# Optimization experiments

Hardware: AMD Instinct MI355X
Metric: run time of the kernel (lower is better)

The kernel has to match this reference:

```python
import jax, jax.numpy as jnp
import numpy as np

B, E, C, Fdim, T = 8, 36, 4, 32, 2048
EDGE_DIM, NODE_DIM, NUM_NODES, NUM_CLASSES = 64, 128, 12, 9
# edges: all (i, j) with i in 0..5, j in 6..11, in loop order
U = np.repeat(np.arange(6), 6)
V = np.tile(np.arange(6, 12), 6)


def _p(key, shape, scale=0.05):
    return jax.random.normal(key, shape, jnp.float32) * scale


def setup_inputs():
    ks = iter(jax.random.split(jax.random.key(0), 64))
    nxt = lambda: next(ks)
    inp = {}
    inp["x"] = jax.random.normal(nxt(), (B, E, C, Fdim, T), jnp.float32)
    inp["conv1_w"] = _p(nxt(), (16, C, 3, 3)); inp["conv1_b"] = _p(nxt(), (16,))
    inp["bn1_s"] = jnp.ones((16,)); inp["bn1_b"] = jnp.zeros((16,))
    inp["bn1_m"] = jnp.zeros((16,)); inp["bn1_v"] = jnp.ones((16,))
    inp["se1_w1"] = _p(nxt(), (4, 16)); inp["se1_b1"] = _p(nxt(), (4,))
    inp["se1_w2"] = _p(nxt(), (16, 4)); inp["se1_b2"] = _p(nxt(), (16,))
    inp["conv2_w"] = _p(nxt(), (32, 16, 3, 3)); inp["conv2_b"] = _p(nxt(), (32,))
    inp["bn2_s"] = jnp.ones((32,)); inp["bn2_b"] = jnp.zeros((32,))
    inp["bn2_m"] = jnp.zeros((32,)); inp["bn2_v"] = jnp.ones((32,))
    inp["se2_w1"] = _p(nxt(), (8, 32)); inp["se2_b1"] = _p(nxt(), (8,))
    inp["se2_w2"] = _p(nxt(), (32, 8)); inp["se2_b2"] = _p(nxt(), (32,))
    inp["conv3_w"] = _p(nxt(), (64, 32, 3, 3)); inp["conv3_b"] = _p(nxt(), (64,))
    inp["bn3_s"] = jnp.ones((64,)); inp["bn3_b"] = jnp.zeros((64,))
    inp["bn3_m"] = jnp.zeros((64,)); inp["bn3_v"] = jnp.ones((64,))
    inp["edge_fc_w"] = _p(nxt(), (EDGE_DIM, 64)); inp["edge_fc_b"] = _p(nxt(), (EDGE_DIM,))
    inp["edge_w"] = _p(nxt(), (E,), 1.0)  # learnable_edge_weights
    inp["e2n_w"] = _p(nxt(), (NODE_DIM, EDGE_DIM)); inp["e2n_b"] = _p(nxt(), (NODE_DIM,))
    inp["attn1_w"] = _p(nxt(), (NODE_DIM // 2, NODE_DIM)); inp["attn1_b"] = _p(nxt(), (NODE_DIM // 2,))
    inp["attn2_w"] = _p(nxt(), (1, NODE_DIM // 2))
    inp["cls_w"] = _p(nxt(), (NUM_CLASSES, NODE_DIM)); inp["cls_b"] = _p(nxt(), (NUM_CLASSES,))
    inp["reg_w"] = _p(nxt(), (3, NODE_DIM)); inp["reg_b"] = _p(nxt(), (3,))
    return inp


def _conv(x, w, b, stride):
    y = jax.lax.conv_general_dilated(x, w, window_strides=stride,
        padding=[(1, 1), (1, 1)], dimension_numbers=("NCHW", "OIHW", "NCHW"))
    return y + b[None, :, None, None]


def _bn(x, s, b, m, v):
    # eval-mode BatchNorm2d (running stats)
    inv = s * jax.lax.rsqrt(v + 1e-5)
    return (x - m[None, :, None, None]) * inv[None, :, None, None] + b[None, :, None, None]


def _maxpool2(x):
    return jax.lax.reduce_window(x, -jnp.inf, jax.lax.max,
        (1, 1, 2, 2), (1, 1, 2, 2), "VALID")


def _se(x, w1, b1, w2, b2):
    y = x.mean(axis=(2, 3))                      # [N, C]
    y = jax.nn.relu(y @ w1.T + b1)
    y = jax.nn.sigmoid(y @ w2.T + b2)
    return x * y[:, :, None, None]


def _forward(x, conv1_w, conv1_b, bn1_s, bn1_b, bn1_m, bn1_v,
             se1_w1, se1_b1, se1_w2, se1_b2,
             conv2_w, conv2_b, bn2_s, bn2_b, bn2_m, bn2_v,
             se2_w1, se2_b1, se2_w2, se2_b2,
             conv3_w, conv3_b, bn3_s, bn3_b, bn3_m, bn3_v,
             edge_fc_w, edge_fc_b, edge_w, e2n_w, e2n_b,
             attn1_w, attn1_b, attn2_w, cls_w, cls_b, reg_w, reg_b):
    h = x.reshape(B * E, C, Fdim, T)
    h = jax.nn.relu(_bn(_conv(h, conv1_w, conv1_b, (1, 2)), bn1_s, bn1_b, bn1_m, bn1_v))
    h = _se(_maxpool2(h), se1_w1, se1_b1, se1_w2, se1_b2)
    h = jax.nn.relu(_bn(_conv(h, conv2_w, conv2_b, (1, 2)), bn2_s, bn2_b, bn2_m, bn2_v))
    h = _se(_maxpool2(h), se2_w1, se2_b1, se2_w2, se2_b2)
    h = jax.nn.relu(_bn(_conv(h, conv3_w, conv3_b, (1, 2)), bn3_s, bn3_b, bn3_m, bn3_v))
    h = h.mean(axis=(2, 3))                      # AdaptiveAvgPool2d(1) -> [B*E, 64]
    edge_feat = jax.nn.relu(h @ edge_fc_w.T + edge_fc_b).reshape(B, E, EDGE_DIM)

    # spatial GNN: weighted edge feats scatter-added to both endpoints
    w = jax.nn.softplus(edge_w)[None, :, None]   # [1, E, 1]
    wef = edge_feat * w                          # [B, E, D]
    node = jnp.zeros((B, NUM_NODES, EDGE_DIM), edge_feat.dtype)
    node = node.at[:, U].add(wef).at[:, V].add(wef)
    node = jax.nn.relu(node @ e2n_w.T + e2n_b)   # [B, 12, NODE_DIM]

    # attention pooling
    scores = jnp.tanh(node @ attn1_w.T + attn1_b) @ attn2_w.T   # [B, 12, 1]
    aw = jax.nn.softmax(scores, axis=1)
    ea = aw[:, U, 0] * aw[:, V, 0]               # [B, E]
    ea = ea / (ea.sum(axis=1, keepdims=True) + 1e-8)
    g = (node * aw).sum(axis=1)                  # [B, NODE_DIM]
    return (g @ reg_w.T + reg_b, g @ cls_w.T + cls_b, ea)


def reference(x, conv1_w, conv1_b, bn1_s, bn1_b, bn1_m, bn1_v,
              se1_w1, se1_b1, se1_w2, se1_b2,
              conv2_w, conv2_b, bn2_s, bn2_b, bn2_m, bn2_v,
              se2_w1, se2_b1, se2_w2, se2_b2,
              conv3_w, conv3_b, bn3_s, bn3_b, bn3_m, bn3_v,
              edge_fc_w, edge_fc_b, edge_w, e2n_w, e2n_b,
              attn1_w, attn1_b, attn2_w, cls_w, cls_b, reg_w, reg_b):
    return _forward(x, conv1_w, conv1_b, bn1_s, bn1_b, bn1_m, bn1_v,
                    se1_w1, se1_b1, se1_w2, se1_b2,
                    conv2_w, conv2_b, bn2_s, bn2_b, bn2_m, bn2_v,
                    se2_w1, se2_b1, se2_w2, se2_b2,
                    conv3_w, conv3_b, bn3_s, bn3_b, bn3_m, bn3_v,
                    edge_fc_w, edge_fc_b, edge_w, e2n_w, e2n_b,
                    attn1_w, attn1_b, attn2_w, cls_w, cls_b, reg_w, reg_b)
```

## Files before the change

kernel.cpp:

```cpp
#include <hip/hip_runtime.h>
#include <math.h>


#define GLOAD_LDS(src, dst) \
  __builtin_amdgcn_global_load_lds( \
      (const __attribute__((address_space(1))) void*)(src), \
      (__attribute__((address_space(3))) void*)(dst), 16, 0, 0)

__global__ __launch_bounds__(256) void k_conv1(
    const float* __restrict__ x, const float* __restrict__ w,
    const float* __restrict__ cb, const float* __restrict__ bs,
    const float* __restrict__ bb, const float* __restrict__ bm,
    const float* __restrict__ bv,
    float* __restrict__ h1, float* __restrict__ sesum)
{
  int bid = blockIdx.x;
  int colq = bid & 3, chunk = (bid >> 2) & 1, n = bid >> 3;
  __shared__ float tile[4][6][520];
  __shared__ float wl[4][3][3][16];
  __shared__ float bi[16];

  const float* xn = x + (size_t)n * 4 * 32 * 2048;
  const int cbase = colq * 512;
  int tid = threadIdx.x;
  for (int i = tid; i < 576; i += 256) {
    int co = i / 36, r = i % 36, ci = r / 9, kk = r % 9;
    float s = bs[co] * rsqrtf(bv[co] + 1e-5f);
    wl[ci][kk / 3][kk % 3][co] = w[i] * s;
  }
  if (tid < 16) {
    int c = tid;
    float s = bs[c] * rsqrtf(bv[c] + 1e-5f);
    bi[c] = bb[c] + (cb[c] - bm[c]) * s;
  }
  int wv = tid >> 6, l = tid & 63;
  const int P0 = chunk * 8;
  {
#pragma unroll
    for (int j = 0; j < 8; j++) {
      int idx = wv * 8 + j;
      int ci = idx >> 3, rowidx = (idx >> 1) & 3, half = idx & 1;
      int ih = 2 * P0 - 1 + rowidx;
      int slot = ((ih % 6) + 6) % 6;
      int ihc = min(max(ih, 0), 31);
      const float* src =
          xn + ((size_t)ci * 32 + ihc) * 2048 + cbase + half * 256 + 4 * l;
      GLOAD_LDS(src, &tile[ci][slot][4 + half * 256 + 4 * l]);
    }
    if (tid < 16) {
      int ri = tid & 3, ci = tid >> 2;
      int ih2 = 2 * P0 - 1 + ri, slot2 = ((ih2 % 6) + 6) % 6;
      int ihc2 = min(max(ih2, 0), 31);
      tile[ci][slot2][3] =
          colq ? xn[((size_t)ci * 32 + ihc2) * 2048 + cbase - 1] : 0.f;
    }
  }
  __syncthreads();

  int cog = tid >> 7, tl = tid & 127;
  int cob = cog * 8;
  float sloc[8] = {0.f, 0.f, 0.f, 0.f, 0.f, 0.f, 0.f, 0.f};

#pragma unroll 1
  for (int pl = 0; pl < 8; pl++) {
    int p = P0 + pl;
    if (pl < 7) {
#pragma unroll
      for (int j = 0; j < 4; j++) {
        int idx = wv * 4 + j;
        int ci = idx >> 2, rsel = (idx >> 1) & 1, half = idx & 1;
        int ih = 2 * p + 3 + rsel;
        int slot = ih % 6;
        int ihc = min(ih, 31);
        const float* src =
            xn + ((size_t)ci * 32 + ihc) * 2048 + cbase + half * 256 + 4 * l;
        GLOAD_LDS(src, &tile[ci][slot][4 + half * 256 + 4 * l]);
      }
      if (tid < 8) {
        int rs2 = tid & 1, ci2 = tid >> 1;
        int ih2 = 2 * p + 3 + rs2, slot2 = ih2 % 6, ihc2 = min(ih2, 31);
        tile[ci2][slot2][3] =
            colq ? xn[((size_t)ci2 * 32 + ihc2) * 2048 + cbase - 1] : 0.f;
      }
    }
    float acc[2][2][8];
#pragma unroll
    for (int cr = 0; cr < 2; cr++)
#pragma unroll
      for (int cc = 0; cc < 2; cc++)
#pragma unroll
        for (int k = 0; k < 8; k++) acc[cr][cc][k] = 0.f;
    const bool ok0 = (p > 0), ok3 = (p < 15);
    int slots[4];
#pragma unroll
    for (int r = 0; r < 4; r++) {
      int ih = 2 * p - 1 + r;
      slots[r] = ((ih % 6) + 6) % 6;
    }
#pragma unroll 1
    for (int ci = 0; ci < 4; ci++) {
      float strip[4][5];
#pragma unroll
      for (int r = 0; r < 4; r++) {
        bool ok = (r == 0) ? ok0 : ((r == 3) ? ok3 : true);
        if (ok) {
          float4 vA = *reinterpret_cast<const float4*>(&tile[ci][slots[r]][4 * tl]);
          float4 vB = *reinterpret_cast<const float4*>(&tile[ci][slots[r]][4 * tl + 4]);
          strip[r][0] = vA.w;
          strip[r][1] = vB.x; strip[r][2] = vB.y; strip[r][3] = vB.z; strip[r][4] = vB.w;
        } else {
          strip[r][0] = strip[r][1] = strip[r][2] = strip[r][3] = strip[r][4] = 0.f;
        }
      }
#pragma unroll
      for (int kh = 0; kh < 3; kh++) {
#pragma unroll
        for (int kw = 0; kw < 3; kw++) {
          const float4* wp = reinterpret_cast<const float4*>(&wl[ci][kh][kw][cob]);
          float4 w0 = wp[0], w1 = wp[1];
          float wr[8] = {w0.x, w0.y, w0.z, w0.w, w1.x, w1.y, w1.z, w1.w};
#pragma unroll
          for (int cr = 0; cr < 2; cr++) {
            float v0 = strip[cr + kh][kw], v1 = strip[cr + kh][2 + kw];
#pragma unroll
            for (int k = 0; k < 8; k++) {
              acc[cr][0][k] = fmaf(v0, wr[k], acc[cr][0][k]);
              acc[cr][1][k] = fmaf(v1, wr[k], acc[cr][1][k]);
            }
          }
        }
      }
    }
    int pc = colq * 128 + tl;
#pragma unroll
    for (int k = 0; k < 8; k++) {
      float m = fmaxf(fmaxf(acc[0][0][k], acc[0][1][k]),
                      fmaxf(acc[1][0][k], acc[1][1][k]));
      float po = fmaxf(m + bi[cob + k], 0.f);
      h1[(((size_t)n * 16 + cob + k) * 16 + p) * 512 + pc] = po;
      sloc[k] += po;
    }
    __syncthreads();
  }
#pragma unroll
  for (int k = 0; k < 8; k++) {
    float v = sloc[k];
    for (int off = 32; off; off >>= 1) v += __shfl_down(v, off);
    if (l == 0) atomicAdd(&sesum[n * 16 + cob + k], v);
  }
}

__global__ void k_se(const float* __restrict__ sesum, int C, int Cr, float invcnt,
                     const float* __restrict__ w1, const float* __restrict__ b1,
                     const float* __restrict__ w2, const float* __restrict__ b2,
                     float* __restrict__ s)
{
  int n = blockIdx.x * blockDim.x + threadIdx.x;
  if (n >= 288) return;
  float y[32], t[8];
  for (int c = 0; c < C; c++) y[c] = sesum[n * C + c] * invcnt;
  for (int r = 0; r < Cr; r++) {
    float a = b1[r];
    for (int c = 0; c < C; c++) a += y[c] * w1[r * C + c];
    t[r] = fmaxf(a, 0.f);
  }
  for (int c = 0; c < C; c++) {
    float a = b2[c];
    for (int r = 0; r < Cr; r++) a += t[r] * w2[c * Cr + r];
    s[n * C + c] = 1.f / (1.f + expf(-a));
  }
}

__global__ __launch_bounds__(256) void k_conv2(
    const float* __restrict__ h1, const float* __restrict__ w,
    const float* __restrict__ cb, const float* __restrict__ bs,
    const float* __restrict__ bb, const float* __restrict__ bm,
    const float* __restrict__ bv,
    const float* __restrict__ s1,
    float* __restrict__ h2, float* __restrict__ sesum)
{
  int bid = blockIdx.x;
  int ph = bid & 7, n = bid >> 3;
  __shared__ float tile[2][2][4][520];
  __shared__ float wl[16][3][3][32];
  __shared__ float bi[32];

  const float* s1n = s1 + n * 16;
  for (int i = threadIdx.x; i < 4608; i += 256) {
    int co = i / 144, r = i % 144, ci = r / 9, kk = r % 9;
    float s = bs[co] * rsqrtf(bv[co] + 1e-5f);
    wl[ci][kk / 3][kk % 3][co] = w[i] * s * s1n[ci];
  }
  if (threadIdx.x < 32) {
    int c = threadIdx.x;
    float s = bs[c] * rsqrtf(bv[c] + 1e-5f);
    bi[c] = bb[c] + (cb[c] - bm[c]) * s;
  }
  if (threadIdx.x < 64) {
    int b = threadIdx.x >> 5, ci = (threadIdx.x >> 4) & 1,
        r = (threadIdx.x >> 2) & 3, k = threadIdx.x & 3;
    tile[b][ci][r][k] = 0.f;
  }

  const float* hn = h1 + (size_t)n * 16 * 16 * 512;
  int wv = threadIdx.x >> 6, l = threadIdx.x & 63;

  auto stage = [&](int c, int b) {
#pragma unroll
    for (int j = 0; j < 4; j++) {
      int idx = 4 * wv + j;
      int ci_l = idx >> 3, r = (idx >> 1) & 3, half = idx & 1;
      int ci = 2 * c + ci_l;
      int ih = min(max(2 * ph - 1 + r, 0), 15);
      const float* src = hn + ((size_t)ci * 16 + ih) * 512 + half * 256 + 4 * l;
      GLOAD_LDS(src, &tile[b][ci_l][r][4 + half * 256 + 4 * l]);
    }
  };

  stage(0, 0);
  __syncthreads();

  int cog = threadIdx.x >> 7, tl = threadIdx.x & 127;
  int cob = cog * 16;
  const bool ok0 = (ph > 0), ok3 = (ph < 7);
  float acc[2][2][16];
#pragma unroll
  for (int cr = 0; cr < 2; cr++)
#pragma unroll
    for (int cc = 0; cc < 2; cc++)
#pragma unroll
      for (int k = 0; k < 16; k++) acc[cr][cc][k] = 0.f;

#pragma unroll 1
  for (int c = 0; c < 8; c++) {
    if (c < 7) stage(c + 1, (c + 1) & 1);
    const int b = c & 1;
#pragma unroll 1
    for (int ci_l = 0; ci_l < 2; ci_l++) {
      int cg = 2 * c + ci_l;
      float strip[4][5];
#pragma unroll
      for (int r = 0; r < 4; r++) {
        bool ok = (r == 0) ? ok0 : ((r == 3) ? ok3 : true);
        if (ok) {
          float4 vA = *reinterpret_cast<const float4*>(&tile[b][ci_l][r][4 * tl]);
          float4 vB = *reinterpret_cast<const float4*>(&tile[b][ci_l][r][4 * tl + 4]);
          strip[r][0] = vA.w;
          strip[r][1] = vB.x; strip[r][2] = vB.y; strip[r][3] = vB.z; strip[r][4] = vB.w;
        } else {
          strip[r][0] = strip[r][1] = strip[r][2] = strip[r][3] = strip[r][4] = 0.f;
        }
      }
#pragma unroll
      for (int kh = 0; kh < 3; kh++) {
#pragma unroll
        for (int kw = 0; kw < 3; kw++) {
          const float4* wp = reinterpret_cast<const float4*>(&wl[cg][kh][kw][cob]);
          float4 w0 = wp[0], w1 = wp[1], w2 = wp[2], w3 = wp[3];
          float wr[16] = {w0.x, w0.y, w0.z, w0.w, w1.x, w1.y, w1.z, w1.w,
                          w2.x, w2.y, w2.z, w2.w, w3.x, w3.y, w3.z, w3.w};
#pragma unroll
          for (int cr = 0; cr < 2; cr++) {
            float v0 = strip[cr + kh][kw], v1 = strip[cr + kh][2 + kw];
#pragma unroll
            for (int k = 0; k < 16; k++) {
              acc[cr][0][k] = fmaf(v0, wr[k], acc[cr][0][k]);
              acc[cr][1][k] = fmaf(v1, wr[k], acc[cr][1][k]);
            }
          }
        }
      }
    }
    if (c < 7) __syncthreads();
  }

#pragma unroll
  for (int k = 0; k < 16; k++) {
    float m = fmaxf(fmaxf(acc[0][0][k], acc[0][1][k]),
                    fmaxf(acc[1][0][k], acc[1][1][k]));
    float po = fmaxf(m + bi[cob + k], 0.f);
    h2[(((size_t)n * 32 + cob + k) * 8 + ph) * 128 + tl] = po;
    float v = po;
    for (int off = 32; off; off >>= 1) v += __shfl_down(v, off);
    if (l == 0) atomicAdd(&sesum[n * 32 + cob + k], v);
  }
}

__global__ __launch_bounds__(256) void k_conv3(
    const float* __restrict__ h2, const float* __restrict__ w,
    const float* __restrict__ cb, const float* __restrict__ bs,
    const float* __restrict__ bb, const float* __restrict__ bm,
    const float* __restrict__ bv,
    const float* __restrict__ s2, float* __restrict__ h3)
{
  int bid = blockIdx.x;
  int n = bid >> 2, cog = bid & 3;
  int hh = threadIdx.x >> 5, t = threadIdx.x & 31;
  __shared__ float tile[8][8][128];
  __shared__ float wl[32][3][3][16];
  __shared__ float bi[16];
  __shared__ float red[4][16];
  const float* s2n = s2 + n * 32;
  for (int i = threadIdx.x; i < 4608; i += 256) {
    int k = i / 288, r = i % 288, ci = r / 9, kk = r % 9;
    int co = cog * 16 + k;
    float s = bs[co] * rsqrtf(bv[co] + 1e-5f);
    wl[ci][kk / 3][kk % 3][k] = w[(size_t)co * 288 + r] * s * s2n[ci];
  }
  if (threadIdx.x < 16) {
    int c = cog * 16 + threadIdx.x;
    float s = bs[c] * rsqrtf(bv[c] + 1e-5f);
    bi[threadIdx.x] = bb[c] + (cb[c] - bm[c]) * s;
  }
  const float* hn = h2 + (size_t)n * 32 * 8 * 128;
  int wv = threadIdx.x >> 6, l = threadIdx.x & 63;
  const int aoff = t ? 4 * t - 4 : 0;
  float acc[2][16];
#pragma unroll
  for (int cc = 0; cc < 2; cc++)
#pragma unroll
    for (int k = 0; k < 16; k++) acc[cc][k] = 0.f;

#pragma unroll 1
  for (int c = 0; c < 4; c++) {
    for (int i = 0; i < 8; i++) {
      int pair = wv * 8 + i;
      int ci_l = pair >> 2, r2 = (pair & 3) * 2;
      int ci = c * 8 + ci_l;
      const float* src = hn + ((size_t)ci * 8 + r2) * 128 + 4 * l;
      GLOAD_LDS(src, &tile[ci_l][r2][4 * l]);
    }
    __syncthreads();
#pragma unroll 1
    for (int ci_l = 0; ci_l < 8; ci_l++) {
      int cg = c * 8 + ci_l;
      float strip[3][5];
#pragma unroll
      for (int r = 0; r < 3; r++) {
        int ih = hh - 1 + r;
        if (ih >= 0 && ih <= 7) {
          float4 vB = *reinterpret_cast<const float4*>(&tile[ci_l][ih][4 * t]);
          float4 vA = *reinterpret_cast<const float4*>(&tile[ci_l][ih][aoff]);
          strip[r][0] = t ? vA.w : 0.f;
          strip[r][1] = vB.x; strip[r][2] = vB.y; strip[r][3] = vB.z; strip[r][4] = vB.w;
        } else {
          strip[r][0] = strip[r][1] = strip[r][2] = strip[r][3] = strip[r][4] = 0.f;
        }
      }
#pragma unroll
      for (int kh = 0; kh < 3; kh++) {
#pragma unroll
        for (int kw = 0; kw < 3; kw++) {
          const float4* wp = reinterpret_cast<const float4*>(&wl[cg][kh][kw][0]);
          float4 w0 = wp[0], w1 = wp[1], w2 = wp[2], w3 = wp[3];
          float wr[16] = {w0.x, w0.y, w0.z, w0.w, w1.x, w1.y, w1.z, w1.w,
                          w2.x, w2.y, w2.z, w2.w, w3.x, w3.y, w3.z, w3.w};
          float v0 = strip[kh][kw], v1 = strip[kh][2 + kw];
#pragma unroll
          for (int k = 0; k < 16; k++) {
            acc[0][k] = fmaf(v0, wr[k], acc[0][k]);
            acc[1][k] = fmaf(v1, wr[k], acc[1][k]);
          }
        }
      }
    }
    __syncthreads();
  }
#pragma unroll
  for (int k = 0; k < 16; k++)
    acc[0][k] = fmaxf(acc[0][k] + bi[k], 0.f) + fmaxf(acc[1][k] + bi[k], 0.f);
#pragma unroll
  for (int k = 0; k < 16; k++) {
    float v = acc[0][k];
    for (int off = 32; off; off >>= 1) v += __shfl_down(v, off);
    if (l == 0) red[wv][k] = v;
  }
  __syncthreads();
  if (threadIdx.x < 16) {
    int k = threadIdx.x;
    float tt = red[0][k] + red[1][k] + red[2][k] + red[3][k];
    h3[n * 64 + cog * 16 + k] = tt * (1.f / 512.f);
  }
}

__global__ __launch_bounds__(256) void k_head(
    const float* __restrict__ h3,
    const float* __restrict__ efw, const float* __restrict__ efb,
    const float* __restrict__ ew,
    const float* __restrict__ e2nw, const float* __restrict__ e2nb,
    const float* __restrict__ a1w, const float* __restrict__ a1b,
    const float* __restrict__ a2w,
    const float* __restrict__ clsw, const float* __restrict__ clsb,
    const float* __restrict__ regw, const float* __restrict__ regb,
    float* __restrict__ out)
{
  int b = blockIdx.x;
  int tid = threadIdx.x;
  __shared__ float ef[36][64];
  __shared__ float nin[12][64];
  __shared__ float nd[12][128];
  __shared__ float tmp[12][64];
  __shared__ float spw[36], aw[12], scv[12], g[128], ea[36];
  if (tid < 36) {
    float xw = ew[tid];
    spw[tid] = (xw > 20.f) ? xw : log1pf(expf(xw));
  }
  __syncthreads();
  for (int idx = tid; idx < 36 * 64; idx += 256) {
    int e = idx >> 6, d = idx & 63;
    const float* hr = h3 + (size_t)(b * 36 + e) * 64;
    const float* wr = efw + d * 64;
    float a = efb[d];
    for (int k = 0; k < 64; k++) a += hr[k] * wr[k];
    ef[e][d] = fmaxf(a, 0.f) * spw[e];
  }
  __syncthreads();
  for (int idx = tid; idx < 12 * 64; idx += 256) {
    int j = idx >> 6, d = idx & 63;
    float a = 0.f;
    if (j < 6) { for (int i = 0; i < 6; i++) a += ef[j * 6 + i][d]; }
    else       { for (int i = 0; i < 6; i++) a += ef[i * 6 + (j - 6)][d]; }
    nin[j][d] = a;
  }
  __syncthreads();
  for (int idx = tid; idx < 12 * 128; idx += 256) {
    int j = idx >> 7, d = idx & 127;
    const float* wr = e2nw + d * 64;
    float a = e2nb[d];
    for (int k = 0; k < 64; k++) a += nin[j][k] * wr[k];
    nd[j][d] = fmaxf(a, 0.f);
  }
  __syncthreads();
  for (int idx = tid; idx < 12 * 64; idx += 256) {
    int j = idx >> 6, hh = idx & 63;
    const float* wr = a1w + hh * 128;
    float a = a1b[hh];
    for (int k = 0; k < 128; k++) a += nd[j][k] * wr[k];
    tmp[j][hh] = tanhf(a) * a2w[hh];
  }
  __syncthreads();
  if (tid < 12) {
    float a = 0.f;
    for (int h = 0; h < 64; h++) a += tmp[tid][h];
    scv[tid] = a;
  }
  __syncthreads();
  if (tid == 0) {
    float m = scv[0];
    for (int j = 1; j < 12; j++) m = fmaxf(m, scv[j]);
    float s = 0.f;
    for (int j = 0; j < 12; j++) { float z = expf(scv[j] - m); aw[j] = z; s += z; }
    float inv = 1.f / s;
    for (int j = 0; j < 12; j++) aw[j] *= inv;
    float rs = 0.f;
    for (int e = 0; e < 36; e++) { float r = aw[e / 6] * aw[6 + e % 6]; ea[e] = r; rs += r; }
    float inv2 = 1.f / (rs + 1e-8f);
    for (int e = 0; e < 36; e++) ea[e] *= inv2;
  }
  __syncthreads();
  if (tid < 36) out[96 + b * 36 + tid] = ea[tid];
  if (tid < 128) {
    float a = 0.f;
    for (int j = 0; j < 12; j++) a += nd[j][tid] * aw[j];
    g[tid] = a;
  }
  __syncthreads();
  if (tid < 3) {
    const float* wr = regw + tid * 128;
    float a = regb[tid];
    for (int k = 0; k < 128; k++) a += g[k] * wr[k];
    out[b * 3 + tid] = a;
  }
  if (tid >= 64 && tid < 73) {
    int i = tid - 64;
    const float* wr = clsw + i * 128;
    float a = clsb[i];
    for (int k = 0; k < 128; k++) a += g[k] * wr[k];
    out[24 + b * 9 + i] = a;
  }
}

extern "C" void kernel_launch(void* const* d_in, const int* in_sizes, int n_in,
                              void* d_out, int out_size, void* d_ws, size_t ws_size,
                              hipStream_t stream) {
  const float* x      = (const float*)d_in[0];
  const float* c1w    = (const float*)d_in[1];
  const float* c1b    = (const float*)d_in[2];
  const float* bn1s   = (const float*)d_in[3];
  const float* bn1b   = (const float*)d_in[4];
  const float* bn1m   = (const float*)d_in[5];
  const float* bn1v   = (const float*)d_in[6];
  const float* se1w1  = (const float*)d_in[7];
  const float* se1b1  = (const float*)d_in[8];
  const float* se1w2  = (const float*)d_in[9];
  const float* se1b2  = (const float*)d_in[10];
  const float* c2w    = (const float*)d_in[11];
  const float* c2b    = (const float*)d_in[12];
  const float* bn2s   = (const float*)d_in[13];
  const float* bn2b   = (const float*)d_in[14];
  const float* bn2m   = (const float*)d_in[15];
  const float* bn2v   = (const float*)d_in[16];
  const float* se2w1  = (const float*)d_in[17];
  const float* se2b1  = (const float*)d_in[18];
  const float* se2w2  = (const float*)d_in[19];
  const float* se2b2  = (const float*)d_in[20];
  const float* c3w    = (const float*)d_in[21];
  const float* c3b    = (const float*)d_in[22];
  const float* bn3s   = (const float*)d_in[23];
  const float* bn3b   = (const float*)d_in[24];
  const float* bn3m   = (const float*)d_in[25];
  const float* bn3v   = (const float*)d_in[26];
  const float* efw    = (const float*)d_in[27];
  const float* efb    = (const float*)d_in[28];
  const float* ew     = (const float*)d_in[29];
  const float* e2nw   = (const float*)d_in[30];
  const float* e2nb   = (const float*)d_in[31];
  const float* a1w    = (const float*)d_in[32];
  const float* a1b    = (const float*)d_in[33];
  const float* a2w    = (const float*)d_in[34];
  const float* clsw   = (const float*)d_in[35];
  const float* clsb   = (const float*)d_in[36];
  const float* regw   = (const float*)d_in[37];
  const float* regb   = (const float*)d_in[38];

  float* ws = (float*)d_ws;
  float* h1     = ws;
  float* h2     = h1 + 37748736;
  float* sesum1 = h2 + 9437184;
  float* s1     = sesum1 + 4608;
  float* sesum2 = s1 + 4608;
  float* s2     = sesum2 + 9216;
  float* h3     = s2 + 9216;

  hipMemsetAsync(sesum1, 0, 4608 * sizeof(float), stream);
  hipMemsetAsync(sesum2, 0, 9216 * sizeof(float), stream);

  k_conv1<<<288 * 8, 256, 0, stream>>>(x, c1w, c1b, bn1s, bn1b, bn1m, bn1v, h1, sesum1);
  k_se<<<5, 64, 0, stream>>>(sesum1, 16, 4, 1.f / 8192.f, se1w1, se1b1, se1w2, se1b2, s1);
  k_conv2<<<288 * 8, 256, 0, stream>>>(h1, c2w, c2b, bn2s, bn2b, bn2m, bn2v, s1, h2, sesum2);
  k_se<<<5, 64, 0, stream>>>(sesum2, 32, 8, 1.f / 1024.f, se2w1, se2b1, se2w2, se2b2, s2);
  k_conv3<<<288 * 4, 256, 0, stream>>>(h2, c3w, c3b, bn3s, bn3b, bn3m, bn3v, s2, h3);
  k_head<<<8, 256, 0, stream>>>(h3, efw, efb, ew, e2nw, e2nb, a1w, a1b, a2w,
                                clsw, clsb, regw, regb, (float*)d_out);
}
```

Baseline: 521.4 us.

## Precompute folded conv weights in global memory and read them as uniform scalar loads

Moves the BN/SE weight folding for conv1 and conv2 out of every block into small prologue kernels that write the folded weights to workspace once (per batch for conv2). The conv kernels then read the weights directly from global memory through a wave-uniform base (readfirstlane) so the compiler can use scalar loads, instead of staging them into LDS. This removes per-block redundant folding work and LDS weight traffic, and frees LDS, at the cost of two extra kernel launches and reliance on the scalar cache for weight reads.

```diff
diff --git a/kernel.cpp b/kernel.cpp
--- a/kernel.cpp
+++ b/kernel.cpp
@@ -7,8 +7,32 @@
       (const __attribute__((address_space(1))) void*)(src), \
       (__attribute__((address_space(3))) void*)(dst), 16, 0, 0)
 
+__global__ void k_fold1(const float* __restrict__ w, const float* __restrict__ bs,
+                        const float* __restrict__ bv, float* __restrict__ wf1)
+{
+  int i = blockIdx.x * blockDim.x + threadIdx.x;
+  if (i < 576) {
+    int co = i / 36, r = i % 36;
+    float s = bs[co] * rsqrtf(bv[co] + 1e-5f);
+    wf1[r * 16 + co] = w[i] * s;
+  }
+}
+
+__global__ void k_fold2(const float* __restrict__ w, const float* __restrict__ bs,
+                        const float* __restrict__ bv, const float* __restrict__ s1,
+                        float* __restrict__ wf2)
+{
+  int n = blockIdx.x;
+  const float* s1n = s1 + n * 16;
+  for (int i = threadIdx.x; i < 4608; i += 256) {
+    int co = i / 144, r = i % 144, ci = r / 9;
+    float s = bs[co] * rsqrtf(bv[co] + 1e-5f);
+    wf2[(size_t)n * 4608 + r * 32 + co] = w[i] * s * s1n[ci];
+  }
+}
+
 __global__ __launch_bounds__(256) void k_conv1(
-    const float* __restrict__ x, const float* __restrict__ w,
+    const float* __restrict__ x, const float* __restrict__ wf1,
     const float* __restrict__ cb, const float* __restrict__ bs,
     const float* __restrict__ bb, const float* __restrict__ bm,
     const float* __restrict__ bv,
@@ -17,17 +41,11 @@
   int bid = blockIdx.x;
   int colq = bid & 3, chunk = (bid >> 2) & 1, n = bid >> 3;
   __shared__ float tile[4][6][520];
-  __shared__ float wl[4][3][3][16];
   __shared__ float bi[16];
 
   const float* xn = x + (size_t)n * 4 * 32 * 2048;
   const int cbase = colq * 512;
   int tid = threadIdx.x;
-  for (int i = tid; i < 576; i += 256) {
-    int co = i / 36, r = i % 36, ci = r / 9, kk = r % 9;
-    float s = bs[co] * rsqrtf(bv[co] + 1e-5f);
-    wl[ci][kk / 3][kk % 3][co] = w[i] * s;
-  }
   if (tid < 16) {
     int c = tid;
     float s = bs[c] * rsqrtf(bv[c] + 1e-5f);
@@ -58,7 +76,7 @@
   __syncthreads();
 
   int cog = tid >> 7, tl = tid & 127;
-  int cob = cog * 8;
+  const int cobu = __builtin_amdgcn_readfirstlane(cog * 8);
   float sloc[8] = {0.f, 0.f, 0.f, 0.f, 0.f, 0.f, 0.f, 0.f};
 
 #pragma unroll 1
@@ -112,12 +130,13 @@
           strip[r][0] = strip[r][1] = strip[r][2] = strip[r][3] = strip[r][4] = 0.f;
         }
       }
+      const float* wci = wf1 + ci * 9 * 16 + cobu;
 #pragma unroll
       for (int kh = 0; kh < 3; kh++) {
 #pragma unroll
         for (int kw = 0; kw < 3; kw++) {
-          const float4* wp = reinterpret_cast<const float4*>(&wl[ci][kh][kw][cob]);
-          float4 w0 = wp[0], w1 = wp[1];
+          const float4* wq = reinterpret_cast<const float4*>(wci + (kh * 3 + kw) * 16);
+          float4 w0 = wq[0], w1 = wq[1];
           float wr[8] = {w0.x, w0.y, w0.z, w0.w, w1.x, w1.y, w1.z, w1.w};
 #pragma unroll
           for (int cr = 0; cr < 2; cr++) {
@@ -136,8 +155,8 @@
     for (int k = 0; k < 8; k++) {
       float m = fmaxf(fmaxf(acc[0][0][k], acc[0][1][k]),
                       fmaxf(acc[1][0][k], acc[1][1][k]));
-      float po = fmaxf(m + bi[cob + k], 0.f);
-      h1[(((size_t)n * 16 + cob + k) * 16 + p) * 512 + pc] = po;
+      float po = fmaxf(m + bi[cobu + k], 0.f);
+      h1[(((size_t)n * 16 + cobu + k) * 16 + p) * 512 + pc] = po;
       sloc[k] += po;
     }
     __syncthreads();
@@ -146,7 +165,7 @@
   for (int k = 0; k < 8; k++) {
     float v = sloc[k];
     for (int off = 32; off; off >>= 1) v += __shfl_down(v, off);
-    if (l == 0) atomicAdd(&sesum[n * 16 + cob + k], v);
+    if (l == 0) atomicAdd(&sesum[n * 16 + cobu + k], v);
   }
 }
 
@@ -172,37 +191,30 @@
 }
 
 __global__ __launch_bounds__(256) void k_conv2(
-    const float* __restrict__ h1, const float* __restrict__ w,
+    const float* __restrict__ h1, const float* __restrict__ wf2,
     const float* __restrict__ cb, const float* __restrict__ bs,
     const float* __restrict__ bb, const float* __restrict__ bm,
     const float* __restrict__ bv,
-    const float* __restrict__ s1,
     float* __restrict__ h2, float* __restrict__ sesum)
 {
   int bid = blockIdx.x;
   int ph = bid & 7, n = bid >> 3;
   __shared__ float tile[2][2][4][520];
-  __shared__ float wl[16][3][3][32];
   __shared__ float bi[32];
 
-  const float* s1n = s1 + n * 16;
-  for (int i = threadIdx.x; i < 4608; i += 256) {
-    int co = i / 144, r = i % 144, ci = r / 9, kk = r % 9;
-    float s = bs[co] * rsqrtf(bv[co] + 1e-5f);
-    wl[ci][kk / 3][kk % 3][co] = w[i] * s * s1n[ci];
-  }
   if (threadIdx.x < 32) {
     int c = threadIdx.x;
     float s = bs[c] * rsqrtf(bv[c] + 1e-5f);
     bi[c] = bb[c] + (cb[c] - bm[c]) * s;
   }
-  if (threadIdx.x < 64) {
-    int b = threadIdx.x >> 5, ci = (threadIdx.x >> 4) & 1,
-        r = (threadIdx.x >> 2) & 3, k = threadIdx.x & 3;
+  if (threadIdx.x >= 64 && threadIdx.x < 128) {
+    int t2 = threadIdx.x - 64;
+    int b = t2 >> 5, ci = (t2 >> 4) & 1, r = (t2 >> 2) & 3, k = t2 & 3;
     tile[b][ci][r][k] = 0.f;
   }
 
   const float* hn = h1 + (size_t)n * 16 * 16 * 512;
+  const float* wfn = wf2 + (size_t)n * 4608;
   int wv = threadIdx.x >> 6, l = threadIdx.x & 63;
 
   auto stage = [&](int c, int b) {
@@ -221,7 +233,7 @@
   __syncthreads();
 
   int cog = threadIdx.x >> 7, tl = threadIdx.x & 127;
-  int cob = cog * 16;
+  const int cobu = __builtin_amdgcn_readfirstlane(cog * 16);
   const bool ok0 = (ph > 0), ok3 = (ph < 7);
   float acc[2][2][16];
 #pragma unroll
@@ -251,12 +263,13 @@
           strip[r][0] = strip[r][1] = strip[r][2] = strip[r][3] = strip[r][4] = 0.f;
         }
       }
+      const float* wci = wfn + cg * 9 * 32 + cobu;
 #pragma unroll
       for (int kh = 0; kh < 3; kh++) {
 #pragma unroll
         for (int kw = 0; kw < 3; kw++) {
-          const float4* wp = reinterpret_cast<const float4*>(&wl[cg][kh][kw][cob]);
-          float4 w0 = wp[0], w1 = wp[1], w2 = wp[2], w3 = wp[3];
+          const float4* wq = reinterpret_cast<const float4*>(wci + (kh * 3 + kw) * 32);
+          float4 w0 = wq[0], w1 = wq[1], w2 = wq[2], w3 = wq[3];
           float wr[16] = {w0.x, w0.y, w0.z, w0.w, w1.x, w1.y, w1.z, w1.w,
                           w2.x, w2.y, w2.z, w2.w, w3.x, w3.y, w3.z, w3.w};
 #pragma unroll
@@ -278,11 +291,11 @@
   for (int k = 0; k < 16; k++) {
     float m = fmaxf(fmaxf(acc[0][0][k], acc[0][1][k]),
                     fmaxf(acc[1][0][k], acc[1][1][k]));
-    float po = fmaxf(m + bi[cob + k], 0.f);
-    h2[(((size_t)n * 32 + cob + k) * 8 + ph) * 128 + tl] = po;
+    float po = fmaxf(m + bi[cobu + k], 0.f);
+    h2[(((size_t)n * 32 + cobu + k) * 8 + ph) * 128 + tl] = po;
     float v = po;
     for (int off = 32; off; off >>= 1) v += __shfl_down(v, off);
-    if (l == 0) atomicAdd(&sesum[n * 32 + cob + k], v);
+    if (l == 0) atomicAdd(&sesum[n * 32 + cobu + k], v);
   }
 }
 
@@ -531,13 +544,17 @@
   float* sesum2 = s1 + 4608;
   float* s2     = sesum2 + 9216;
   float* h3     = s2 + 9216;
+  float* wf1    = h3 + 18432;
+  float* wf2    = wf1 + 576;
 
   hipMemsetAsync(sesum1, 0, 4608 * sizeof(float), stream);
   hipMemsetAsync(sesum2, 0, 9216 * sizeof(float), stream);
 
-  k_conv1<<<288 * 8, 256, 0, stream>>>(x, c1w, c1b, bn1s, bn1b, bn1m, bn1v, h1, sesum1);
+  k_fold1<<<3, 192, 0, stream>>>(c1w, bn1s, bn1v, wf1);
+  k_conv1<<<288 * 8, 256, 0, stream>>>(x, wf1, c1b, bn1s, bn1b, bn1m, bn1v, h1, sesum1);
   k_se<<<5, 64, 0, stream>>>(sesum1, 16, 4, 1.f / 8192.f, se1w1, se1b1, se1w2, se1b2, s1);
-  k_conv2<<<288 * 8, 256, 0, stream>>>(h1, c2w, c2b, bn2s, bn2b, bn2m, bn2v, s1, h2, sesum2);
+  k_fold2<<<288, 256, 0, stream>>>(c2w, bn2s, bn2v, s1, wf2);
+  k_conv2<<<288 * 8, 256, 0, stream>>>(h1, wf2, c2b, bn2s, bn2b, bn2m, bn2v, h2, sesum2);
   k_se<<<5, 64, 0, stream>>>(sesum2, 32, 8, 1.f / 1024.f, se2w1, se2b1, se2w2, se2b2, s2);
   k_conv3<<<288 * 4, 256, 0, stream>>>(h2, c3w, c3b, bn3s, bn3b, bn3m, bn3v, s2, h3);
   k_head<<<8, 256, 0, stream>>>(h3, efw, efb, ew, e2nw, e2nb, a1w, a1b, a2w,
```

Result: faster. 474.7 us (-9.0%).
